# Kernel optimization log

Hardware: AMD Instinct MI355X
Metric: run time of the kernel (lower is better)

## Reference

```python
import jax, jax.numpy as jnp
import numpy as np

EPS = 1e-5

def conv1x1(x, w):
    # x: [B,C,T,D,H,W], w: [O,C] -> [B,O,T,D,H,W]
    return jnp.einsum('oc,bctdhw->botdhw', w, x)

def conv4d_3(x, w):
    # 3x3x3x3 4D conv, padding=1, stride=1, decomposed as 3 shifted 3D convs.
    # x: [B,C,T,D,H,W], w: [O,C,3,3,3,3]
    B, C, T, D, H, W = x.shape
    O = w.shape[0]
    xp = jnp.pad(x, ((0, 0), (0, 0), (1, 1), (1, 1), (1, 1), (1, 1)))
    out = None
    for k in range(3):  # small fixed loop over first kernel dim
        xk = xp[:, :, k:k + T]                      # [B,C,T,D+2,H+2,W+2]
        xk = xk.transpose(0, 2, 1, 3, 4, 5).reshape(B * T, C, D + 2, H + 2, W + 2)
        ok = jax.lax.conv_general_dilated(
            xk, w[:, :, k], window_strides=(1, 1, 1), padding='VALID',
            dimension_numbers=('NCDHW', 'OIDHW', 'NCDHW'))  # [B*T,O,D,H,W]
        out = ok if out is None else out + ok
    return out.reshape(B, T, O, D, H, W).transpose(0, 2, 1, 3, 4, 5)

def bn4d(x, g, b):
    # BatchNorm over (B, T, D, H, W) per channel (training-mode batch stats).
    axes = (0, 2, 3, 4, 5)
    m = jnp.mean(x, axis=axes, keepdims=True)
    v = jnp.mean(jnp.square(x - m), axis=axes, keepdims=True)
    sh = (1, -1, 1, 1, 1, 1)
    return (x - m) * jax.lax.rsqrt(v + EPS) * g.reshape(sh) + b.reshape(sh)

def setup_inputs() -> dict:
    key = jax.random.key(0)
    ks = jax.random.split(key, 4)
    B, C, T, D, H, W = 2, 256, 8, 16, 16, 16
    planes = 64
    return {
        'x': jax.random.normal(ks[0], (B, C, T, D, H, W), jnp.float32),
        'w1': jax.random.normal(ks[1], (planes, C), jnp.float32) * 0.05,
        'g1': jnp.ones((planes,), jnp.float32),
        'b1': jnp.zeros((planes,), jnp.float32),
        'w2': jax.random.normal(ks[2], (planes, planes, 3, 3, 3, 3), jnp.float32) * 0.05,
        'g2': jnp.ones((planes,), jnp.float32),
        'b2': jnp.zeros((planes,), jnp.float32),
        'w3': jax.random.normal(ks[3], (4 * planes, planes), jnp.float32) * 0.05,
        'g3': jnp.ones((4 * planes,), jnp.float32),
        'b3': jnp.zeros((4 * planes,), jnp.float32),
    }

def reference(x, w1, g1, b1, w2, g2, b2, w3, g3, b3):
    out = jax.nn.relu(bn4d(conv1x1(x, w1), g1, b1))
    out = jax.nn.relu(bn4d(conv4d_3(out, w2), g2, b2))
    out = bn4d(conv1x1(out, w3), g3, b3)
    return jax.nn.relu(out + x)
```

## Files before the change

kernel.cpp:

```cpp
#include <hip/hip_runtime.h>

#define S_TOT 32768

typedef unsigned short ushortT;
typedef __attribute__((ext_vector_type(8))) short short8;
typedef __attribute__((ext_vector_type(4))) float floatx4;

__device__ __forceinline__ ushortT f2bf(float f) {
    unsigned u = __float_as_uint(f);
    u = (u + 0x7fffu + ((u >> 16) & 1u)) >> 16;
    return (ushortT)u;
}
__device__ __forceinline__ float bf2f(ushortT h) {
    return __uint_as_float(((unsigned)h) << 16);
}

__global__ __launch_bounds__(256) void k_prep_w(const float* __restrict__ w1,
                                                const float* __restrict__ w2,
                                                const float* __restrict__ w3,
                                                ushortT* __restrict__ wb1,
                                                ushortT* __restrict__ wb2,
                                                ushortT* __restrict__ wb3) {
    int idx = blockIdx.x * 256 + threadIdx.x;
    if (idx < 16384) {
        int e = idx;
        int j = e & 7, o = (e >> 3) & 63, q = (e >> 9) & 3, cc = e >> 11;
        int c = cc * 32 + q * 8 + j;
        wb1[e] = f2bf(w1[o * 256 + c]);
    } else if (idx < 16384 + 331776) {
        int e = idx - 16384;
        int j = e & 7, o = (e >> 3) & 63, cb = (e >> 9) & 7, tap = e >> 12;
        int c = cb * 8 + j;
        wb2[e] = f2bf(w2[((size_t)o * 64 + c) * 81 + tap]);
    } else if (idx < 16384 + 331776 + 16384) {
        int e = idx - 348160;
        int j = e & 7, o = (e >> 3) & 255, g = e >> 11;
        int ks = g >> 2, q = g & 3;
        int c = ks * 32 + q * 8 + j;
        wb3[e] = f2bf(w3[o * 64 + c]);
    }
}

__global__ __launch_bounds__(256) void k_stats_bf16(const ushortT* __restrict__ y,
                                                    int nch,
                                                    float* __restrict__ sum,
                                                    float* __restrict__ sq) {
    __shared__ float red[8];
    int ch = blockIdx.x, tid = threadIdx.x;
    float s = 0.f, q = 0.f;
    for (int b = 0; b < 2; ++b) {
        const ushortT* p = y + ((size_t)(b * nch + ch)) * S_TOT;
        for (int i = tid * 8; i < S_TOT; i += 256 * 8) {
            uint4 v = *(const uint4*)(p + i);
            uint32_t va[4] = {v.x, v.y, v.z, v.w};
#pragma unroll
            for (int k = 0; k < 4; ++k) {
                float a = bf2f((ushortT)(va[k] & 0xffffu));
                float c = bf2f((ushortT)(va[k] >> 16));
                s += a + c;
                q += a * a + c * c;
            }
        }
    }
#pragma unroll
    for (int off = 32; off; off >>= 1) {
        s += __shfl_down(s, off);
        q += __shfl_down(q, off);
    }
    int wid = tid >> 6;
    if ((tid & 63) == 0) { red[wid] = s; red[4 + wid] = q; }
    __syncthreads();
    if (tid == 0) {
        sum[ch] = red[0] + red[1] + red[2] + red[3];
        sq[ch]  = red[4] + red[5] + red[6] + red[7];
    }
}

__global__ __launch_bounds__(256) void k_stats_f32(const float* __restrict__ y,
                                                   int nch,
                                                   float* __restrict__ sum,
                                                   float* __restrict__ sq) {
    __shared__ float red[8];
    int ch = blockIdx.x, tid = threadIdx.x;
    float s = 0.f, q = 0.f;
    for (int b = 0; b < 2; ++b) {
        const float* p = y + ((size_t)(b * nch + ch)) * S_TOT;
        for (int i = tid * 4; i < S_TOT; i += 256 * 4) {
            float4 v = *(const float4*)(p + i);
            s += v.x + v.y + v.z + v.w;
            q += v.x * v.x + v.y * v.y + v.z * v.z + v.w * v.w;
        }
    }
#pragma unroll
    for (int off = 32; off; off >>= 1) {
        s += __shfl_down(s, off);
        q += __shfl_down(q, off);
    }
    int wid = tid >> 6;
    if ((tid & 63) == 0) { red[wid] = s; red[4 + wid] = q; }
    __syncthreads();
    if (tid == 0) {
        sum[ch] = red[0] + red[1] + red[2] + red[3];
        sq[ch]  = red[4] + red[5] + red[6] + red[7];
    }
}

__global__ __launch_bounds__(256) void k_conv1_mfma(const float* __restrict__ x,
                                                    const ushortT* __restrict__ wb1,
                                                    ushortT* __restrict__ y1bf) {
    __shared__ __align__(16) ushortT xb[128 * 40];

    int tid = threadIdx.x;
    int blk = blockIdx.x;
    int b  = blk >> 8;
    int n0 = (blk & 255) * 128;

    int lane = tid & 63;
    int wv   = tid >> 6;
    int m    = lane & 15;
    int q    = lane >> 4;

    int c_loc = tid & 31;
    int ng    = tid >> 5;

    floatx4 acc[8];
#pragma unroll
    for (int i = 0; i < 8; ++i) acc[i] = (floatx4){0.f, 0.f, 0.f, 0.f};

    for (int cc = 0; cc < 8; ++cc) {
        short8 afr = *(const short8*)(wb1 + (((cc * 4 + q) * 64) + wv * 16 + m) * 8);

        __syncthreads();
        {
            int c = cc * 32 + c_loc;
            const float* xp = x + ((size_t)(b * 256 + c)) * S_TOT + n0 + ng * 16;
#pragma unroll
            for (int k = 0; k < 4; ++k) {
                float4 v = *(const float4*)(xp + k * 4);
                int nb = ng * 16 + k * 4;
                xb[(nb + 0) * 40 + c_loc] = f2bf(v.x);
                xb[(nb + 1) * 40 + c_loc] = f2bf(v.y);
                xb[(nb + 2) * 40 + c_loc] = f2bf(v.z);
                xb[(nb + 3) * 40 + c_loc] = f2bf(v.w);
            }
        }
        __syncthreads();

#pragma unroll
        for (int pt = 0; pt < 8; ++pt) {
            short8 bfr = *(const short8*)(xb + (pt * 16 + m) * 40 + q * 8);
            acc[pt] = __builtin_amdgcn_mfma_f32_16x16x32_bf16(afr, bfr, acc[pt], 0, 0, 0);
        }
    }

#pragma unroll
    for (int pt = 0; pt < 8; ++pt) {
#pragma unroll
        for (int r = 0; r < 4; ++r) {
            int o = wv * 16 + q * 4 + r;
            y1bf[((size_t)(b * 64 + o)) * S_TOT + n0 + pt * 16 + m] = f2bf(acc[pt][r]);
        }
    }
}

__global__ __launch_bounds__(256) void k_prep(const ushortT* __restrict__ yin,
                                              const float* __restrict__ sum,
                                              const float* __restrict__ sq,
                                              const float* __restrict__ g,
                                              const float* __restrict__ bb,
                                              ushortT* __restrict__ yout) {
    size_t i = ((size_t)blockIdx.x * 256 + threadIdx.x) * 4;
    int c = (int)((i >> 15) & 63);
    const float n = 65536.f;
    float mean = sum[c] / n;
    float var  = sq[c] / n - mean * mean;
    float a  = g[c] * rsqrtf(var + 1e-5f);
    float bs = bb[c] - mean * a;
    ushort4 v = *(const ushort4*)(yin + i);
    ushort4 r;
    r.x = f2bf(fmaxf(a * bf2f(v.x) + bs, 0.f));
    r.y = f2bf(fmaxf(a * bf2f(v.y) + bs, 0.f));
    r.z = f2bf(fmaxf(a * bf2f(v.z) + bs, 0.f));
    r.w = f2bf(fmaxf(a * bf2f(v.w) + bs, 0.f));
    *(ushort4*)(yout + i) = r;
}

__global__ __launch_bounds__(256, 2) void k_conv2_mfma(
        const ushortT* __restrict__ y1n,
        const ushortT* __restrict__ wb2,
        ushortT* __restrict__ y2bf) {
    __shared__ __align__(16) ushortT xs[180 * 72];

    int tid = threadIdx.x;
    int blk = blockIdx.x;
    int b  = blk >> 8;
    int t  = (blk >> 5) & 7;
    int d  = (blk >> 1) & 15;
    int h0 = (blk & 1) * 8;

    int lane = tid & 63;
    int wv   = tid >> 6;
    int m    = lane & 15;
    int q    = lane >> 4;

    int c2      = tid & 31;
    int prbase  = tid >> 5;

    floatx4 acc[8];
#pragma unroll
    for (int i = 0; i < 8; ++i) acc[i] = (floatx4){0.f, 0.f, 0.f, 0.f};

    const size_t cstride = 32768;
    uint32_t* xsd = (uint32_t*)xs;

    for (int ktd = 0; ktd < 9; ++ktd) {
        int kt = ktd / 3, kd = ktd - kt * 3;
        int tt = t + kt - 1;
        int dd = d + kd - 1;
        bool pv = (tt >= 0 && tt < 8 && dd >= 0 && dd < 16);

        short8 afr[9][2];
#pragma unroll
        for (int khw = 0; khw < 9; ++khw) {
#pragma unroll
            for (int ks = 0; ks < 2; ++ks) {
                int tap = ktd * 9 + khw;
                const ushortT* wp =
                    wb2 + (((size_t)(tap * 8 + ks * 4 + q)) * 64 + wv * 16 + m) * 8;
                afr[khw][ks] = *(const short8*)wp;
            }
        }

        __syncthreads();

        for (int pr = prbase; pr < 10; pr += 8) {
            int hin = h0 + pr - 1;
            uint32_t pack[18];
            if (pv && hin >= 0 && hin < 16) {
                const ushortT* p0 = y1n +
                    (((size_t)(b * 64 + 2 * c2) * 8 + tt) * 16 + dd) * 256 + hin * 16;
                const ushortT* p1 = p0 + cstride;
                uint4 r0 = *(const uint4*)p0;
                uint4 r1 = *(const uint4*)(p0 + 8);
                uint4 s0 = *(const uint4*)p1;
                uint4 s1 = *(const uint4*)(p1 + 8);
                uint32_t ra[8] = {r0.x, r0.y, r0.z, r0.w, r1.x, r1.y, r1.z, r1.w};
                uint32_t sa[8] = {s0.x, s0.y, s0.z, s0.w, s1.x, s1.y, s1.z, s1.w};
                pack[0] = 0; pack[17] = 0;
#pragma unroll
                for (int k = 0; k < 8; ++k) {
                    pack[1 + 2 * k] = (ra[k] & 0xffffu) | (sa[k] << 16);
                    pack[2 + 2 * k] = (ra[k] >> 16) | (sa[k] & 0xffff0000u);
                }
            } else {
#pragma unroll
                for (int k = 0; k < 18; ++k) pack[k] = 0;
            }
            int base = pr * 18 * 36 + c2;
#pragma unroll
            for (int k = 0; k < 18; ++k) xsd[base + k * 36] = pack[k];
        }
        __syncthreads();

#pragma unroll
        for (int khw = 0; khw < 9; ++khw) {
            int kh = khw / 3, kw = khw - kh * 3;
#pragma unroll
            for (int nt = 0; nt < 8; ++nt) {
                int ppos = (nt + kh) * 18 + m + kw;
                const ushortT* bp = xs + ppos * 72 + q * 8;
                short8 b0 = *(const short8*)bp;
                short8 b1 = *(const short8*)(bp + 32);
                acc[nt] = __builtin_amdgcn_mfma_f32_16x16x32_bf16(
                    afr[khw][0], b0, acc[nt], 0, 0, 0);
                acc[nt] = __builtin_amdgcn_mfma_f32_16x16x32_bf16(
                    afr[khw][1], b1, acc[nt], 0, 0, 0);
            }
        }
    }

#pragma unroll
    for (int nt = 0; nt < 8; ++nt) {
#pragma unroll
        for (int r = 0; r < 4; ++r) {
            int o = wv * 16 + q * 4 + r;
            y2bf[(((size_t)(b * 64 + o) * 8 + t) * 16 + d) * 256 + (h0 + nt) * 16 + m] =
                f2bf(acc[nt][r]);
        }
    }
}

__global__ __launch_bounds__(256) void k_conv3_mfma(const ushortT* __restrict__ y2n,
                                                    const ushortT* __restrict__ wb3,
                                                    float* __restrict__ y3) {
    __shared__ __align__(16) ushortT yb[64 * 72];

    int tid = threadIdx.x;
    int blk = blockIdx.x;
    int b  = blk >> 9;
    int n0 = (blk & 511) * 64;

    int lane = tid & 63;
    int wv   = tid >> 6;
    int m    = lane & 15;
    int q    = lane >> 4;

    for (int idx = tid; idx < 512; idx += 256) {
        int c = idx >> 3, k = idx & 7;
        uint4 v = *(const uint4*)(y2n + ((size_t)(b * 64 + c)) * S_TOT + n0 + k * 8);
        uint32_t va[4] = {v.x, v.y, v.z, v.w};
#pragma unroll
        for (int p = 0; p < 4; ++p) {
            yb[(k * 8 + 2 * p)     * 72 + c] = (ushortT)(va[p] & 0xffffu);
            yb[(k * 8 + 2 * p + 1) * 72 + c] = (ushortT)(va[p] >> 16);
        }
    }
    __syncthreads();

    floatx4 acc[4][4];
#pragma unroll
    for (int i = 0; i < 4; ++i)
#pragma unroll
        for (int j = 0; j < 4; ++j) acc[i][j] = (floatx4){0.f, 0.f, 0.f, 0.f};

#pragma unroll
    for (int ks = 0; ks < 2; ++ks) {
        short8 afr[4];
#pragma unroll
        for (int ot = 0; ot < 4; ++ot)
            afr[ot] = *(const short8*)(wb3 +
                (((ks * 4 + q) * 256) + wv * 64 + ot * 16 + m) * 8);
#pragma unroll
        for (int pt = 0; pt < 4; ++pt) {
            short8 bfr = *(const short8*)(yb + (pt * 16 + m) * 72 + ks * 32 + q * 8);
#pragma unroll
            for (int ot = 0; ot < 4; ++ot)
                acc[ot][pt] = __builtin_amdgcn_mfma_f32_16x16x32_bf16(
                    afr[ot], bfr, acc[ot][pt], 0, 0, 0);
        }
    }

#pragma unroll
    for (int ot = 0; ot < 4; ++ot) {
#pragma unroll
        for (int pt = 0; pt < 4; ++pt) {
#pragma unroll
            for (int r = 0; r < 4; ++r) {
                int o = wv * 64 + ot * 16 + q * 4 + r;
                y3[((size_t)(b * 256 + o)) * S_TOT + n0 + pt * 16 + m] = acc[ot][pt][r];
            }
        }
    }
}

__global__ __launch_bounds__(256) void k_final(const float* __restrict__ x,
                                               const float* __restrict__ sum,
                                               const float* __restrict__ sq,
                                               const float* __restrict__ g,
                                               const float* __restrict__ bb,
                                               float* __restrict__ out) {
    size_t i = ((size_t)blockIdx.x * 256 + threadIdx.x) * 4;
    int o = (int)((i >> 15) & 255);
    const float n = 65536.f;
    float mean = sum[o] / n;
    float var  = sq[o] / n - mean * mean;
    float a  = g[o] * rsqrtf(var + 1e-5f);
    float bs = bb[o] - mean * a;
    float4 y  = *(float4*)(out + i);
    float4 xv = *(const float4*)(x + i);
    float4 r;
    r.x = fmaxf(a * y.x + bs + xv.x, 0.f);
    r.y = fmaxf(a * y.y + bs + xv.y, 0.f);
    r.z = fmaxf(a * y.z + bs + xv.z, 0.f);
    r.w = fmaxf(a * y.w + bs + xv.w, 0.f);
    *(float4*)(out + i) = r;
}

extern "C" void kernel_launch(void* const* d_in, const int* in_sizes, int n_in,
                              void* d_out, int out_size, void* d_ws, size_t ws_size,
                              hipStream_t stream) {
    const float* x  = (const float*)d_in[0];
    const float* w1 = (const float*)d_in[1];
    const float* g1 = (const float*)d_in[2];
    const float* b1 = (const float*)d_in[3];
    const float* w2 = (const float*)d_in[4];
    const float* g2 = (const float*)d_in[5];
    const float* b2 = (const float*)d_in[6];
    const float* w3 = (const float*)d_in[7];
    const float* g3 = (const float*)d_in[8];
    const float* b3 = (const float*)d_in[9];

    char* ws = (char*)d_ws;
    ushortT* y1bf = (ushortT*)(ws);
    ushortT* y1n  = (ushortT*)(ws + 8388608);
    ushortT* y2bf = (ushortT*)(ws + 16777216);
    ushortT* y2n  = (ushortT*)(ws + 25165824);
    ushortT* wb1  = (ushortT*)(ws + 33554432);
    ushortT* wb2  = (ushortT*)(ws + 33587200);
    ushortT* wb3  = (ushortT*)(ws + 34250752);
    float*   stats = (float*)(ws + 34283520);
    float* sum1 = stats;        float* sq1 = stats + 64;
    float* sum2 = stats + 128;  float* sq2 = stats + 192;
    float* sum3 = stats + 256;  float* sq3 = stats + 512;
    float* y3 = (float*)d_out;

    k_prep_w     <<<1424,  256, 0, stream>>>(w1, w2, w3, wb1, wb2, wb3);
    k_conv1_mfma <<<512,   256, 0, stream>>>(x, wb1, y1bf);
    k_stats_bf16 <<<64,    256, 0, stream>>>(y1bf, 64, sum1, sq1);
    k_prep       <<<4096,  256, 0, stream>>>(y1bf, sum1, sq1, g1, b1, y1n);
    k_conv2_mfma <<<512,   256, 0, stream>>>(y1n, wb2, y2bf);
    k_stats_bf16 <<<64,    256, 0, stream>>>(y2bf, 64, sum2, sq2);
    k_prep       <<<4096,  256, 0, stream>>>(y2bf, sum2, sq2, g2, b2, y2n);
    k_conv3_mfma <<<1024,  256, 0, stream>>>(y2n, wb3, y3);
    k_stats_f32  <<<256,   256, 0, stream>>>(y3, 256, sum3, sq3);
    k_final      <<<16384, 256, 0, stream>>>(x, sum3, sq3, g3, b3, y3);
}
```

Before: 267.7 us.

## Retile conv2 MFMA waves to 2x2 output/position split with swizzled LDS

Conv2 waves now each own 32 output channels by 4 spatial rows instead of 16 channels by 8 rows. Each B fragment read from LDS is therefore reused across two output tiles, which halves shared-memory read traffic per MFMA. The LDS layout drops the 72-element padding in favour of an XOR swizzle to avoid bank conflicts. Time slices whose shifted input lies entirely in padding are skipped, removing their loads and MFMAs. The cost is twice the A-fragment registers per wave, which may pressure occupancy.

```diff
diff --git a/kernel.cpp b/kernel.cpp
--- a/kernel.cpp
+++ b/kernel.cpp
@@ -189,7 +189,7 @@
         const ushortT* __restrict__ y1n,
         const ushortT* __restrict__ wb2,
         ushortT* __restrict__ y2bf) {
-    __shared__ __align__(16) ushortT xs[180 * 72];
+    __shared__ __align__(16) ushortT xs[180 * 64];
 
     int tid = threadIdx.x;
     int blk = blockIdx.x;
@@ -202,13 +202,17 @@
     int wv   = tid >> 6;
     int m    = lane & 15;
     int q    = lane >> 4;
+    int wp   = wv & 1;
+    int wo   = wv >> 1;
 
     int c2      = tid & 31;
     int prbase  = tid >> 5;
 
-    floatx4 acc[8];
-#pragma unroll
-    for (int i = 0; i < 8; ++i) acc[i] = (floatx4){0.f, 0.f, 0.f, 0.f};
+    floatx4 acc[2][4];
+#pragma unroll
+    for (int i = 0; i < 2; ++i)
+#pragma unroll
+        for (int j = 0; j < 4; ++j) acc[i][j] = (floatx4){0.f, 0.f, 0.f, 0.f};
 
     const size_t cstride = 32768;
     uint32_t* xsd = (uint32_t*)xs;
@@ -218,17 +222,19 @@
         int tt = t + kt - 1;
         int dd = d + kd - 1;
         bool pv = (tt >= 0 && tt < 8 && dd >= 0 && dd < 16);
-
-        short8 afr[9][2];
+        if (!pv) continue;
+
+        short8 afr[9][2][2];
 #pragma unroll
         for (int khw = 0; khw < 9; ++khw) {
-#pragma unroll
-            for (int ks = 0; ks < 2; ++ks) {
-                int tap = ktd * 9 + khw;
-                const ushortT* wp =
-                    wb2 + (((size_t)(tap * 8 + ks * 4 + q)) * 64 + wv * 16 + m) * 8;
-                afr[khw][ks] = *(const short8*)wp;
-            }
+            int tap = ktd * 9 + khw;
+#pragma unroll
+            for (int ks = 0; ks < 2; ++ks)
+#pragma unroll
+                for (int ot = 0; ot < 2; ++ot) {
+                    afr[khw][ks][ot] = *(const short8*)(wb2 +
+                        (((size_t)(tap * 8 + ks * 4 + q)) * 64 + wo * 32 + ot * 16 + m) * 8);
+                }
         }
 
         __syncthreads();
@@ -236,7 +242,7 @@
         for (int pr = prbase; pr < 10; pr += 8) {
             int hin = h0 + pr - 1;
             uint32_t pack[18];
-            if (pv && hin >= 0 && hin < 16) {
+            if (hin >= 0 && hin < 16) {
                 const ushortT* p0 = y1n +
                     (((size_t)(b * 64 + 2 * c2) * 8 + tt) * 16 + dd) * 256 + hin * 16;
                 const ushortT* p1 = p0 + cstride;
@@ -256,36 +262,51 @@
 #pragma unroll
                 for (int k = 0; k < 18; ++k) pack[k] = 0;
             }
-            int base = pr * 18 * 36 + c2;
-#pragma unroll
-            for (int k = 0; k < 18; ++k) xsd[base + k * 36] = pack[k];
+            int pb = pr * 18;
+#pragma unroll
+            for (int k = 0; k < 18; ++k) {
+                int ppos = pb + k;
+                xsd[ppos * 32 + ((((c2 >> 2) ^ (ppos & 7)) << 2) | (c2 & 3))] = pack[k];
+            }
         }
         __syncthreads();
 
 #pragma unroll
-        for (int khw = 0; khw < 9; ++khw) {
-            int kh = khw / 3, kw = khw - kh * 3;
-#pragma unroll
-            for (int nt = 0; nt < 8; ++nt) {
-                int ppos = (nt + kh) * 18 + m + kw;
-                const ushortT* bp = xs + ppos * 72 + q * 8;
-                short8 b0 = *(const short8*)bp;
-                short8 b1 = *(const short8*)(bp + 32);
-                acc[nt] = __builtin_amdgcn_mfma_f32_16x16x32_bf16(
-                    afr[khw][0], b0, acc[nt], 0, 0, 0);
-                acc[nt] = __builtin_amdgcn_mfma_f32_16x16x32_bf16(
-                    afr[khw][1], b1, acc[nt], 0, 0, 0);
-            }
-        }
-    }
-
-#pragma unroll
-    for (int nt = 0; nt < 8; ++nt) {
-#pragma unroll
-        for (int r = 0; r < 4; ++r) {
-            int o = wv * 16 + q * 4 + r;
-            y2bf[(((size_t)(b * 64 + o) * 8 + t) * 16 + d) * 256 + (h0 + nt) * 16 + m] =
-                f2bf(acc[nt][r]);
+        for (int kh = 0; kh < 3; ++kh) {
+#pragma unroll
+            for (int kw = 0; kw < 3; ++kw) {
+                int khw = kh * 3 + kw;
+#pragma unroll
+                for (int nt = 0; nt < 4; ++nt) {
+                    int ppos = (wp * 4 + nt + kh) * 18 + m + kw;
+                    int sw = (ppos & 7);
+                    const ushortT* row = xs + ppos * 64;
+                    short8 b0 = *(const short8*)(row + (((0 * 4 + q) ^ sw) << 3));
+                    short8 b1 = *(const short8*)(row + (((1 * 4 + q) ^ sw) << 3));
+                    acc[0][nt] = __builtin_amdgcn_mfma_f32_16x16x32_bf16(
+                        afr[khw][0][0], b0, acc[0][nt], 0, 0, 0);
+                    acc[1][nt] = __builtin_amdgcn_mfma_f32_16x16x32_bf16(
+                        afr[khw][0][1], b0, acc[1][nt], 0, 0, 0);
+                    acc[0][nt] = __builtin_amdgcn_mfma_f32_16x16x32_bf16(
+                        afr[khw][1][0], b1, acc[0][nt], 0, 0, 0);
+                    acc[1][nt] = __builtin_amdgcn_mfma_f32_16x16x32_bf16(
+                        afr[khw][1][1], b1, acc[1][nt], 0, 0, 0);
+                }
+            }
+        }
+    }
+
+#pragma unroll
+    for (int ot = 0; ot < 2; ++ot) {
+#pragma unroll
+        for (int nt = 0; nt < 4; ++nt) {
+#pragma unroll
+            for (int r = 0; r < 4; ++r) {
+                int o  = wo * 32 + ot * 16 + q * 4 + r;
+                int hh = h0 + wp * 4 + nt;
+                y2bf[(((size_t)(b * 64 + o) * 8 + t) * 16 + d) * 256 + hh * 16 + m] =
+                    f2bf(acc[ot][nt][r]);
+            }
         }
     }
 }
```

Result: no change. 269.9 us (+0.8%).
